# Optimization experiments

Hardware: AMD Instinct MI355X
Metric: run time of the kernel (lower is better)

Reference implementation:

```python
import jax, jax.numpy as jnp
import numpy as np

D = 768
N_GROUPS = 4
KEYS_PER_Q = 4 * 196  # 784


def setup_inputs() -> dict:
    key = jax.random.key(0)
    ks = jax.random.split(key, 6)
    scale = 0.02
    return {
        "LR_image": jax.random.normal(ks[0], (N_GROUPS, 32, D), jnp.float32),
        "HR_image": jax.random.normal(ks[1], (N_GROUPS, 32 * KEYS_PER_Q, D), jnp.float32),
        "Wq": jax.random.normal(ks[2], (D, D), jnp.float32) * scale,
        "bq": jnp.zeros((D,), jnp.float32),
        "Wk": jax.random.normal(ks[3], (D, D), jnp.float32) * scale,
        "bk": jnp.zeros((D,), jnp.float32),
        "Wv": jax.random.normal(ks[4], (D, D), jnp.float32) * scale,
        "bv": jnp.zeros((D,), jnp.float32),
        "Wo": jax.random.normal(ks[5], (D, D), jnp.float32) * scale,
        "bo": jnp.zeros((D,), jnp.float32),
        "gamma": jnp.ones((D,), jnp.float32),
        "beta": jnp.zeros((D,), jnp.float32),
    }


def reference(LR_image, HR_image, Wq, bq, Wk, bk, Wv, bv, Wo, bo, gamma, beta):
    d = LR_image.shape[-1]
    # version == 2 reshapes from the original forward
    lr = LR_image.reshape(1, -1, 32, 1, d)            # [1, N, 32, 1, D]
    hr = HR_image.reshape(1, -1, 32, KEYS_PER_Q, d)   # [1, N, 32, 784, D]
    q = lr @ Wq.T + bq                                # [1, N, 32, 1, D]
    k = hr @ Wk.T + bk                                # [1, N, 32, 784, D]
    v = hr @ Wv.T + bv
    # single-head attention; query_len == 1, key_len == 784
    scores = jnp.einsum('bnsqd,bnskd->bnsqk', q, k) / jnp.sqrt(jnp.float32(d))
    p = jax.nn.softmax(scores, axis=-1)               # dropout = identity (eval)
    x = jnp.einsum('bnsqk,bnskd->bnsqd', p, v)        # [1, N, 32, 1, D]
    x = x.reshape(1, -1, d)                           # [1, N*32, D]
    q = q.reshape(1, -1, d)
    x = x @ Wo.T + bo
    y = q + x                                         # residual (dropout_2 = identity)
    mu = jnp.mean(y, axis=-1, keepdims=True)
    var = jnp.mean((y - mu) ** 2, axis=-1, keepdims=True)
    return (y - mu) * jax.lax.rsqrt(var + 1e-5) * gamma + beta
```

## Files before the change

### kernel.cpp

```cpp
#include <hip/hip_runtime.h>
#include <math.h>

#define D 768
#define DF2 384
#define DF4 192
#define NQ 128
#define KPQ 784
#define NCHUNK 16
#define KCHUNK 49

#define EXP2F(x) __builtin_amdgcn_exp2f(x)

__device__ __forceinline__ float dot4f(const float4 a, const float4 b) {
    return a.x * b.x + a.y * b.y + a.z * b.z + a.w * b.w;
}

__global__ __launch_bounds__(256) void k_tr(const float* __restrict__ Wq,
                                            const float* __restrict__ Wv,
                                            const float* __restrict__ Wo,
                                            float* __restrict__ WqT,
                                            float* __restrict__ WvT,
                                            float* __restrict__ WoT) {
    __shared__ float t[64][65];
    const float* src;
    float* dst;
    if (blockIdx.y == 0)      { src = Wq; dst = WqT; }
    else if (blockIdx.y == 1) { src = Wv; dst = WvT; }
    else                      { src = Wo; dst = WoT; }
    const int tr = blockIdx.x / 12, tc = blockIdx.x % 12;
    const int r0 = tr * 64, c0 = tc * 64;
    const int lr = threadIdx.x >> 6, lc = threadIdx.x & 63;
#pragma unroll
    for (int i = 0; i < 16; ++i)
        t[lr + i * 4][lc] = src[(size_t)(r0 + lr + i * 4) * D + c0 + lc];
    __syncthreads();
#pragma unroll
    for (int i = 0; i < 16; ++i)
        dst[(size_t)(c0 + lr + i * 4) * D + r0 + lc] = t[lc][lr + i * 4];
}

template <bool BIAS, bool RES>
__global__ __launch_bounds__(512) void k_gemm2(const float* __restrict__ A,
                                               const float2* __restrict__ W2,
                                               const float2* __restrict__ bias2,
                                               const float2* __restrict__ res2,
                                               float2* __restrict__ Out2) {
    __shared__ float2 part[8][4][64];
    const int ct  = blockIdx.x % 6;
    const int q0  = (blockIdx.x / 6) * 4;
    const int tid = threadIdx.x;
    const int ds  = __builtin_amdgcn_readfirstlane(tid >> 6);
    const int c2  = tid & 63;
    const int e2  = ct * 64 + c2;
    const float* a0 = A + (size_t)q0 * D;
    const float* a1 = a0 + D;
    const float* a2 = a1 + D;
    const float* a3 = a2 + D;
    float2 acc0 = {0.f, 0.f}, acc1 = {0.f, 0.f}, acc2 = {0.f, 0.f}, acc3 = {0.f, 0.f};
    const int dbase = ds * 96;
#pragma unroll 8
    for (int i = 0; i < 96; ++i) {
        const int d = dbase + i;
        const float2 wv = W2[(size_t)d * DF2 + e2];
        const float x0 = a0[d], x1 = a1[d], x2 = a2[d], x3 = a3[d];
        acc0.x = fmaf(x0, wv.x, acc0.x); acc0.y = fmaf(x0, wv.y, acc0.y);
        acc1.x = fmaf(x1, wv.x, acc1.x); acc1.y = fmaf(x1, wv.y, acc1.y);
        acc2.x = fmaf(x2, wv.x, acc2.x); acc2.y = fmaf(x2, wv.y, acc2.y);
        acc3.x = fmaf(x3, wv.x, acc3.x); acc3.y = fmaf(x3, wv.y, acc3.y);
    }
    part[ds][0][c2] = acc0;
    part[ds][1][c2] = acc1;
    part[ds][2][c2] = acc2;
    part[ds][3][c2] = acc3;
    __syncthreads();
    if (tid < 256) {
        const int q = tid >> 6, c = tid & 63;
        float2 s = {0.f, 0.f};
#pragma unroll
        for (int p = 0; p < 8; ++p) {
            s.x += part[p][q][c].x;
            s.y += part[p][q][c].y;
        }
        if (BIAS) {
            const float2 b = bias2[ct * 64 + c];
            s.x += b.x; s.y += b.y;
        }
        if (RES) {
            const float2 r = res2[(size_t)(q0 + q) * DF2 + ct * 64 + c];
            s.x += r.x; s.y += r.y;
        }
        Out2[(size_t)(q0 + q) * DF2 + ct * 64 + c] = s;
    }
}

__global__ __launch_bounds__(256) void k_flash(const float4* __restrict__ HR,
                                               const float4* __restrict__ qt,
                                               float4* __restrict__ Cpart,
                                               float2* __restrict__ ML) {
    const int b     = blockIdx.x;
    const int qi    = b >> 4;
    const int chunk = b & 15;
    const size_t rowbase = (size_t)qi * KPQ + (size_t)chunk * KCHUNK;
    const int tid  = threadIdx.x;
    const int w    = tid >> 6;
    const int lane = tid & 63;

    const float rsd2 = 0.036084391824351615f * 1.4426950408889634f;
    float4 qa = qt[qi * DF4 + lane];
    float4 qb = qt[qi * DF4 + lane + 64];
    float4 qc = qt[qi * DF4 + lane + 128];
    qa.x *= rsd2; qa.y *= rsd2; qa.z *= rsd2; qa.w *= rsd2;
    qb.x *= rsd2; qb.y *= rsd2; qb.z *= rsd2; qb.w *= rsd2;
    qc.x *= rsd2; qc.y *= rsd2; qc.z *= rsd2; qc.w *= rsd2;

    float m = -1e30f, l = 0.f;
    float4 c0 = make_float4(0.f, 0.f, 0.f, 0.f);
    float4 c1 = make_float4(0.f, 0.f, 0.f, 0.f);
    float4 c2 = make_float4(0.f, 0.f, 0.f, 0.f);

    int j = w;
    while (j + 4 < KCHUNK) {
        const float4* rowA = HR + (rowbase + (size_t)j) * DF4;
        const float4* rowB = HR + (rowbase + (size_t)(j + 4)) * DF4;
        const float4 a0 = rowA[lane], a1 = rowA[lane + 64], a2 = rowA[lane + 128];
        const float4 b0 = rowB[lane], b1 = rowB[lane + 64], b2 = rowB[lane + 128];
        float p1 = dot4f(qa, a0) + dot4f(qb, a1) + dot4f(qc, a2);
        float p2 = dot4f(qa, b0) + dot4f(qb, b1) + dot4f(qc, b2);
#pragma unroll
        for (int off = 32; off; off >>= 1) {
            p1 += __shfl_xor(p1, off, 64);
            p2 += __shfl_xor(p2, off, 64);
        }
        const float mn = fmaxf(m, fmaxf(p1, p2));
        const float ea = EXP2F(m - mn);
        const float e1 = EXP2F(p1 - mn);
        const float e2 = EXP2F(p2 - mn);
        l = l * ea + e1 + e2;
        c0.x = fmaf(c0.x, ea, fmaf(e1, a0.x, e2 * b0.x));
        c0.y = fmaf(c0.y, ea, fmaf(e1, a0.y, e2 * b0.y));
        c0.z = fmaf(c0.z, ea, fmaf(e1, a0.z, e2 * b0.z));
        c0.w = fmaf(c0.w, ea, fmaf(e1, a0.w, e2 * b0.w));
        c1.x = fmaf(c1.x, ea, fmaf(e1, a1.x, e2 * b1.x));
        c1.y = fmaf(c1.y, ea, fmaf(e1, a1.y, e2 * b1.y));
        c1.z = fmaf(c1.z, ea, fmaf(e1, a1.z, e2 * b1.z));
        c1.w = fmaf(c1.w, ea, fmaf(e1, a1.w, e2 * b1.w));
        c2.x = fmaf(c2.x, ea, fmaf(e1, a2.x, e2 * b2.x));
        c2.y = fmaf(c2.y, ea, fmaf(e1, a2.y, e2 * b2.y));
        c2.z = fmaf(c2.z, ea, fmaf(e1, a2.z, e2 * b2.z));
        c2.w = fmaf(c2.w, ea, fmaf(e1, a2.w, e2 * b2.w));
        m = mn;
        j += 8;
    }
    if (j < KCHUNK) {
        const float4* rowA = HR + (rowbase + (size_t)j) * DF4;
        const float4 a0 = rowA[lane], a1 = rowA[lane + 64], a2 = rowA[lane + 128];
        float p1 = dot4f(qa, a0) + dot4f(qb, a1) + dot4f(qc, a2);
#pragma unroll
        for (int off = 32; off; off >>= 1) p1 += __shfl_xor(p1, off, 64);
        const float mn = fmaxf(m, p1);
        const float ea = EXP2F(m - mn);
        const float e1 = EXP2F(p1 - mn);
        l = l * ea + e1;
        c0.x = fmaf(c0.x, ea, e1 * a0.x); c0.y = fmaf(c0.y, ea, e1 * a0.y);
        c0.z = fmaf(c0.z, ea, e1 * a0.z); c0.w = fmaf(c0.w, ea, e1 * a0.w);
        c1.x = fmaf(c1.x, ea, e1 * a1.x); c1.y = fmaf(c1.y, ea, e1 * a1.y);
        c1.z = fmaf(c1.z, ea, e1 * a1.z); c1.w = fmaf(c1.w, ea, e1 * a1.w);
        c2.x = fmaf(c2.x, ea, e1 * a2.x); c2.y = fmaf(c2.y, ea, e1 * a2.y);
        c2.z = fmaf(c2.z, ea, e1 * a2.z); c2.w = fmaf(c2.w, ea, e1 * a2.w);
        m = mn;
    }

    __shared__ __align__(16) float4 c_lds[4][DF4];
    __shared__ float m_lds[4], l_lds[4];
    c_lds[w][lane]       = c0;
    c_lds[w][lane + 64]  = c1;
    c_lds[w][lane + 128] = c2;
    if (lane == 0) { m_lds[w] = m; l_lds[w] = l; }
    __syncthreads();

    if (tid < DF4) {
        float M = fmaxf(fmaxf(m_lds[0], m_lds[1]), fmaxf(m_lds[2], m_lds[3]));
        float L = 0.f;
        float4 cc = make_float4(0.f, 0.f, 0.f, 0.f);
#pragma unroll
        for (int p = 0; p < 4; ++p) {
            const float wg = EXP2F(m_lds[p] - M);
            L += l_lds[p] * wg;
            const float4 cv = c_lds[p][tid];
            cc.x += cv.x * wg; cc.y += cv.y * wg; cc.z += cv.z * wg; cc.w += cv.w * wg;
        }
        Cpart[(size_t)b * DF4 + tid] = cc;
        if (tid == 0) ML[b] = make_float2(M, L);
    }
}

__global__ __launch_bounds__(192) void k_combine(const float4* __restrict__ Cpart,
                                                 const float2* __restrict__ ML,
                                                 float4* __restrict__ Cn) {
    const int qi = blockIdx.x;
    const int f  = threadIdx.x;
    float mmax = -1e30f;
    float2 mls[NCHUNK];
#pragma unroll
    for (int p = 0; p < NCHUNK; ++p) {
        mls[p] = ML[qi * NCHUNK + p];
        mmax = fmaxf(mmax, mls[p].x);
    }
    float L = 0.f;
    float4 c = make_float4(0.f, 0.f, 0.f, 0.f);
#pragma unroll
    for (int p = 0; p < NCHUNK; ++p) {
        const float wg = EXP2F(mls[p].x - mmax);
        L += mls[p].y * wg;
        const float4 v = Cpart[(size_t)(qi * NCHUNK + p) * DF4 + f];
        c.x += v.x * wg; c.y += v.y * wg; c.z += v.z * wg; c.w += v.w * wg;
    }
    const float inv = 1.f / L;
    c.x *= inv; c.y *= inv; c.z *= inv; c.w *= inv;
    Cn[(size_t)qi * DF4 + f] = c;
}

__global__ __launch_bounds__(256) void k_ln(const float* __restrict__ y,
                                            const float* __restrict__ gamma,
                                            const float* __restrict__ beta,
                                            float* __restrict__ out) {
    __shared__ float sp[4], ssp[4];
    const int qi = blockIdx.x;
    const int tid = threadIdx.x, w = tid >> 6, lane = tid & 63;
    const float* yr = y + (size_t)qi * D;
    const float v0 = yr[tid], v1 = yr[tid + 256], v2 = yr[tid + 512];
    float s  = v0 + v1 + v2;
    float ss = v0 * v0 + v1 * v1 + v2 * v2;
#pragma unroll
    for (int off = 32; off; off >>= 1) {
        s  += __shfl_xor(s, off, 64);
        ss += __shfl_xor(ss, off, 64);
    }
    if (lane == 0) { sp[w] = s; ssp[w] = ss; }
    __syncthreads();
    s  = sp[0] + sp[1] + sp[2] + sp[3];
    ss = ssp[0] + ssp[1] + ssp[2] + ssp[3];
    const float mu  = s * (1.f / 768.f);
    const float var = ss * (1.f / 768.f) - mu * mu;
    const float rs  = rsqrtf(var + 1e-5f);
    float* o = out + (size_t)qi * D;
    o[tid]       = (v0 - mu) * rs * gamma[tid]       + beta[tid];
    o[tid + 256] = (v1 - mu) * rs * gamma[tid + 256] + beta[tid + 256];
    o[tid + 512] = (v2 - mu) * rs * gamma[tid + 512] + beta[tid + 512];
}

extern "C" void kernel_launch(void* const* d_in, const int* in_sizes, int n_in,
                              void* d_out, int out_size, void* d_ws, size_t ws_size,
                              hipStream_t stream) {
    const float* LR    = (const float*)d_in[0];
    const float* HR    = (const float*)d_in[1];
    const float* Wq    = (const float*)d_in[2];
    const float* bq    = (const float*)d_in[3];
    const float* Wk    = (const float*)d_in[4];
    const float* Wv    = (const float*)d_in[6];
    const float* bv    = (const float*)d_in[7];
    const float* Wo    = (const float*)d_in[8];
    const float* bo    = (const float*)d_in[9];
    const float* gamma = (const float*)d_in[10];
    const float* beta  = (const float*)d_in[11];
    float* out = (float*)d_out;

    float* ws = (float*)d_ws;
    float* WqT   = ws;
    float* WvT   = ws + 589824;
    float* WoT   = ws + 1179648;
    float* qbuf  = ws + 1769472;
    float* qtbuf = ws + 1867776;
    float* Cpart = ws + 1966080;
    float* ML    = ws + 3538944;
    float* Cn    = ws + 3543040;
    float* Xbuf  = ws + 3641344;
    float* ybuf  = ws + 3739648;

    k_tr<<<dim3(144, 3), 256, 0, stream>>>(Wq, Wv, Wo, WqT, WvT, WoT);
    k_gemm2<true, false><<<192, 512, 0, stream>>>(LR, (const float2*)WqT,
                                                  (const float2*)bq, nullptr,
                                                  (float2*)qbuf);
    k_gemm2<false, false><<<192, 512, 0, stream>>>(qbuf, (const float2*)Wk,
                                                   nullptr, nullptr,
                                                   (float2*)qtbuf);
    k_flash<<<NQ * NCHUNK, 256, 0, stream>>>((const float4*)HR, (const float4*)qtbuf,
                                             (float4*)Cpart, (float2*)ML);
    k_combine<<<NQ, 192, 0, stream>>>((const float4*)Cpart, (const float2*)ML, (float4*)Cn);
    k_gemm2<true, false><<<192, 512, 0, stream>>>(Cn, (const float2*)WvT,
                                                  (const float2*)bv, nullptr,
                                                  (float2*)Xbuf);
    k_gemm2<true, true><<<192, 512, 0, stream>>>(Xbuf, (const float2*)WoT,
                                                 (const float2*)bo, (const float2*)qbuf,
                                                 (float2*)ybuf);
    k_ln<<<NQ, 256, 0, stream>>>(ybuf, gamma, beta, out);
}
```

Baseline: 104.9 us.

## Fuse split-softmax combine into V-projection GEMM and rebalance flash chunks

Removes the separate combine kernel and folds the cross-chunk softmax merge into the Wv projection GEMM. Each block now rebuilds the normalized context rows in shared memory from the per-chunk partials and log-sum-exp data. The flash kernel now splits each query's keys into 14 chunks of 56 instead of 16 of 49, so the loop has a fixed trip count and no tail. Launch grids move to 2D. This saves one launch and the Cn round trip. In exchange, each of the 6 column-tile blocks recomputes the same combine, which means redundant Cpart reads, and the flash grid has fewer blocks.

```diff
diff --git a/kernel.cpp b/kernel.cpp
--- a/kernel.cpp
+++ b/kernel.cpp
@@ -6,8 +6,8 @@
 #define DF4 192
 #define NQ 128
 #define KPQ 784
-#define NCHUNK 16
-#define KCHUNK 49
+#define NCHUNK 14
+#define KCHUNK 56
 
 #define EXP2F(x) __builtin_amdgcn_exp2f(x)
 
@@ -46,8 +46,8 @@
                                                const float2* __restrict__ res2,
                                                float2* __restrict__ Out2) {
     __shared__ float2 part[8][4][64];
-    const int ct  = blockIdx.x % 6;
-    const int q0  = (blockIdx.x / 6) * 4;
+    const int ct  = blockIdx.x;
+    const int q0  = blockIdx.y * 4;
     const int tid = threadIdx.x;
     const int ds  = __builtin_amdgcn_readfirstlane(tid >> 6);
     const int c2  = tid & 63;
@@ -93,13 +93,87 @@
     }
 }
 
+__global__ __launch_bounds__(512) void k_gemmX(const float* __restrict__ Cpart,
+                                               const float2* __restrict__ ML,
+                                               const float2* __restrict__ W2,
+                                               const float2* __restrict__ bias2,
+                                               float2* __restrict__ Out2) {
+    __shared__ float wgn[4][NCHUNK];
+    __shared__ float cn[4][D];
+    __shared__ float2 part[8][4][64];
+    const int ct  = blockIdx.x;
+    const int q0  = blockIdx.y * 4;
+    const int tid = threadIdx.x;
+
+    if (tid < 4 * NCHUNK) {
+        const int q = tid / NCHUNK, p = tid % NCHUNK;
+        float mmax = -1e30f;
+#pragma unroll
+        for (int pp = 0; pp < NCHUNK; ++pp)
+            mmax = fmaxf(mmax, ML[(q0 + q) * NCHUNK + pp].x);
+        float L = 0.f;
+#pragma unroll
+        for (int pp = 0; pp < NCHUNK; ++pp) {
+            const float2 ml = ML[(q0 + q) * NCHUNK + pp];
+            L += ml.y * EXP2F(ml.x - mmax);
+        }
+        const float2 mlp = ML[(q0 + q) * NCHUNK + p];
+        wgn[q][p] = EXP2F(mlp.x - mmax) / L;
+    }
+    __syncthreads();
+
+#pragma unroll
+    for (int r = 0; r < 6; ++r) {
+        const int idx = r * 512 + tid;
+        const int q = idx / D, dd = idx % D;
+        float s = 0.f;
+#pragma unroll
+        for (int p = 0; p < NCHUNK; ++p)
+            s = fmaf(wgn[q][p], Cpart[(size_t)((q0 + q) * NCHUNK + p) * D + dd], s);
+        cn[q][dd] = s;
+    }
+    __syncthreads();
+
+    const int ds  = __builtin_amdgcn_readfirstlane(tid >> 6);
+    const int c2  = tid & 63;
+    const int e2  = ct * 64 + c2;
+    float2 acc0 = {0.f, 0.f}, acc1 = {0.f, 0.f}, acc2 = {0.f, 0.f}, acc3 = {0.f, 0.f};
+    const int dbase = ds * 96;
+#pragma unroll 8
+    for (int i = 0; i < 96; ++i) {
+        const int d = dbase + i;
+        const float2 wv = W2[(size_t)d * DF2 + e2];
+        const float x0 = cn[0][d], x1 = cn[1][d], x2 = cn[2][d], x3 = cn[3][d];
+        acc0.x = fmaf(x0, wv.x, acc0.x); acc0.y = fmaf(x0, wv.y, acc0.y);
+        acc1.x = fmaf(x1, wv.x, acc1.x); acc1.y = fmaf(x1, wv.y, acc1.y);
+        acc2.x = fmaf(x2, wv.x, acc2.x); acc2.y = fmaf(x2, wv.y, acc2.y);
+        acc3.x = fmaf(x3, wv.x, acc3.x); acc3.y = fmaf(x3, wv.y, acc3.y);
+    }
+    part[ds][0][c2] = acc0;
+    part[ds][1][c2] = acc1;
+    part[ds][2][c2] = acc2;
+    part[ds][3][c2] = acc3;
+    __syncthreads();
+    if (tid < 256) {
+        const int q = tid >> 6, c = tid & 63;
+        float2 s = {0.f, 0.f};
+#pragma unroll
+        for (int p = 0; p < 8; ++p) {
+            s.x += part[p][q][c].x;
+            s.y += part[p][q][c].y;
+        }
+        const float2 b = bias2[ct * 64 + c];
+        s.x += b.x; s.y += b.y;
+        Out2[(size_t)(q0 + q) * DF2 + ct * 64 + c] = s;
+    }
+}
+
 __global__ __launch_bounds__(256) void k_flash(const float4* __restrict__ HR,
                                                const float4* __restrict__ qt,
                                                float4* __restrict__ Cpart,
                                                float2* __restrict__ ML) {
-    const int b     = blockIdx.x;
-    const int qi    = b >> 4;
-    const int chunk = b & 15;
+    const int chunk = blockIdx.x;
+    const int qi    = blockIdx.y;
     const size_t rowbase = (size_t)qi * KPQ + (size_t)chunk * KCHUNK;
     const int tid  = threadIdx.x;
     const int w    = tid >> 6;
@@ -118,8 +192,8 @@
     float4 c1 = make_float4(0.f, 0.f, 0.f, 0.f);
     float4 c2 = make_float4(0.f, 0.f, 0.f, 0.f);
 
-    int j = w;
-    while (j + 4 < KCHUNK) {
+    for (int it = 0; it < 7; ++it) {
+        const int j = w + it * 8;
         const float4* rowA = HR + (rowbase + (size_t)j) * DF4;
         const float4* rowB = HR + (rowbase + (size_t)(j + 4)) * DF4;
         const float4 a0 = rowA[lane], a1 = rowA[lane + 64], a2 = rowA[lane + 128];
@@ -149,25 +223,6 @@
         c2.z = fmaf(c2.z, ea, fmaf(e1, a2.z, e2 * b2.z));
         c2.w = fmaf(c2.w, ea, fmaf(e1, a2.w, e2 * b2.w));
         m = mn;
-        j += 8;
-    }
-    if (j < KCHUNK) {
-        const float4* rowA = HR + (rowbase + (size_t)j) * DF4;
-        const float4 a0 = rowA[lane], a1 = rowA[lane + 64], a2 = rowA[lane + 128];
-        float p1 = dot4f(qa, a0) + dot4f(qb, a1) + dot4f(qc, a2);
-#pragma unroll
-        for (int off = 32; off; off >>= 1) p1 += __shfl_xor(p1, off, 64);
-        const float mn = fmaxf(m, p1);
-        const float ea = EXP2F(m - mn);
-        const float e1 = EXP2F(p1 - mn);
-        l = l * ea + e1;
-        c0.x = fmaf(c0.x, ea, e1 * a0.x); c0.y = fmaf(c0.y, ea, e1 * a0.y);
-        c0.z = fmaf(c0.z, ea, e1 * a0.z); c0.w = fmaf(c0.w, ea, e1 * a0.w);
-        c1.x = fmaf(c1.x, ea, e1 * a1.x); c1.y = fmaf(c1.y, ea, e1 * a1.y);
-        c1.z = fmaf(c1.z, ea, e1 * a1.z); c1.w = fmaf(c1.w, ea, e1 * a1.w);
-        c2.x = fmaf(c2.x, ea, e1 * a2.x); c2.y = fmaf(c2.y, ea, e1 * a2.y);
-        c2.z = fmaf(c2.z, ea, e1 * a2.z); c2.w = fmaf(c2.w, ea, e1 * a2.w);
-        m = mn;
     }
 
     __shared__ __align__(16) float4 c_lds[4][DF4];
@@ -189,35 +244,9 @@
             const float4 cv = c_lds[p][tid];
             cc.x += cv.x * wg; cc.y += cv.y * wg; cc.z += cv.z * wg; cc.w += cv.w * wg;
         }
-        Cpart[(size_t)b * DF4 + tid] = cc;
-        if (tid == 0) ML[b] = make_float2(M, L);
-    }
-}
-
-__global__ __launch_bounds__(192) void k_combine(const float4* __restrict__ Cpart,
-                                                 const float2* __restrict__ ML,
-                                                 float4* __restrict__ Cn) {
-    const int qi = blockIdx.x;
-    const int f  = threadIdx.x;
-    float mmax = -1e30f;
-    float2 mls[NCHUNK];
-#pragma unroll
-    for (int p = 0; p < NCHUNK; ++p) {
-        mls[p] = ML[qi * NCHUNK + p];
-        mmax = fmaxf(mmax, mls[p].x);
-    }
-    float L = 0.f;
-    float4 c = make_float4(0.f, 0.f, 0.f, 0.f);
-#pragma unroll
-    for (int p = 0; p < NCHUNK; ++p) {
-        const float wg = EXP2F(mls[p].x - mmax);
-        L += mls[p].y * wg;
-        const float4 v = Cpart[(size_t)(qi * NCHUNK + p) * DF4 + f];
-        c.x += v.x * wg; c.y += v.y * wg; c.z += v.z * wg; c.w += v.w * wg;
-    }
-    const float inv = 1.f / L;
-    c.x *= inv; c.y *= inv; c.z *= inv; c.w *= inv;
-    Cn[(size_t)qi * DF4 + f] = c;
+        Cpart[(size_t)(qi * NCHUNK + chunk) * DF4 + tid] = cc;
+        if (tid == 0) ML[qi * NCHUNK + chunk] = make_float2(M, L);
+    }
 }
 
 __global__ __launch_bounds__(256) void k_ln(const float* __restrict__ y,
@@ -272,26 +301,24 @@
     float* qbuf  = ws + 1769472;
     float* qtbuf = ws + 1867776;
     float* Cpart = ws + 1966080;
-    float* ML    = ws + 3538944;
-    float* Cn    = ws + 3543040;
-    float* Xbuf  = ws + 3641344;
-    float* ybuf  = ws + 3739648;
+    float* ML    = ws + 3342336;
+    float* Xbuf  = ws + 3345920;
+    float* ybuf  = ws + 3444224;
 
     k_tr<<<dim3(144, 3), 256, 0, stream>>>(Wq, Wv, Wo, WqT, WvT, WoT);
-    k_gemm2<true, false><<<192, 512, 0, stream>>>(LR, (const float2*)WqT,
-                                                  (const float2*)bq, nullptr,
-                                                  (float2*)qbuf);
-    k_gemm2<false, false><<<192, 512, 0, stream>>>(qbuf, (const float2*)Wk,
-                                                   nullptr, nullptr,
-                                                   (float2*)qtbuf);
-    k_flash<<<NQ * NCHUNK, 256, 0, stream>>>((const float4*)HR, (const float4*)qtbuf,
-                                             (float4*)Cpart, (float2*)ML);
-    k_combine<<<NQ, 192, 0, stream>>>((const float4*)Cpart, (const float2*)ML, (float4*)Cn);
-    k_gemm2<true, false><<<192, 512, 0, stream>>>(Cn, (const float2*)WvT,
-                                                  (const float2*)bv, nullptr,
-                                                  (float2*)Xbuf);
-    k_gemm2<true, true><<<192, 512, 0, stream>>>(Xbuf, (const float2*)WoT,
-                                                 (const float2*)bo, (const float2*)qbuf,
-                                                 (float2*)ybuf);
+    k_gemm2<true, false><<<dim3(6, 32), 512, 0, stream>>>(LR, (const float2*)WqT,
+                                                          (const float2*)bq, nullptr,
+                                                          (float2*)qbuf);
+    k_gemm2<false, false><<<dim3(6, 32), 512, 0, stream>>>(qbuf, (const float2*)Wk,
+                                                           nullptr, nullptr,
+                                                           (float2*)qtbuf);
+    k_flash<<<dim3(NCHUNK, NQ), 256, 0, stream>>>((const float4*)HR, (const float4*)qtbuf,
+                                                  (float4*)Cpart, (float2*)ML);
+    k_gemmX<<<dim3(6, 32), 512, 0, stream>>>(Cpart, (const float2*)ML,
+                                             (const float2*)WvT, (const float2*)bv,
+                                             (float2*)Xbuf);
+    k_gemm2<true, true><<<dim3(6, 32), 512, 0, stream>>>(Xbuf, (const float2*)WoT,
+                                                         (const float2*)bo, (const float2*)qbuf,
+                                                         (float2*)ybuf);
     k_ln<<<NQ, 256, 0, stream>>>(ybuf, gamma, beta, out);
 }
```

Result: slower. 138.3 us (+31.9%).
